# Kernel tuning notes

Measured on AMD Instinct MI355X. Metric: run time of the kernel, lower is better.

## Reference

```python
import jax, jax.numpy as jnp
import numpy as np

CDECAY = 0.5      # NEURON_CDECAY = 1/2
VDECAY = 0.75     # NEURON_VDECAY = 3/4
VTH_INIT = 0.5
T = 50            # batch_window
sg = jax.lax.stop_gradient


@jax.custom_vjp
def pseudo_spike(v, vth):
    return (v > vth).astype(v.dtype)

def _ps_fwd(v, vth):
    return pseudo_spike(v, vth), (v, vth)

def _ps_bwd(res, g):
    v, vth = res
    # PseudoSpikeRect: rectangular surrogate gradient, window 0.5; no grad to vth
    return (g * (jnp.abs(v - vth) < 0.5).astype(g.dtype), jnp.zeros_like(vth))

pseudo_spike.defvjp(_ps_fwd, _ps_bwd)


def lif_step(x_in, W, b, u, v_prev, s_prev, temporal):
    """One neuron_model_* call + the temporal-threshold update that follows it."""
    u = u * CDECAY + x_in @ W.T + b
    v = v_prev * VDECAY * (1.0 - s_prev) + u
    # energy threshold term uses detached volts in the original (numpy round-trip)
    energy = jnp.exp((sg(v_prev) - sg(v)) / 3.0) - 1.0
    vth = 0.5 * temporal + 0.5 * energy
    s = pseudo_spike(v, vth)
    vsg = sg(v)  # threshold chain never reaches the loss (custom fn has no vth grad)
    V_m = vsg.mean() - 0.2 * (vsg.max() - vsg.min())
    V_theta = vth.mean() - 0.2 * (vth.max() - vth.min())
    temporal_new = 0.01 * (vsg - V_m) + V_theta + jnp.log(1.0 + jnp.exp((vsg - V_m) / 4.0))
    return u, v, s, temporal_new


def _forward(x, fc1_u, fc1_v, fc1_s, fc2_u, fc2_v, fc2_s, fc3_u, fc3_v, fc3_s,
             fc4_u, fc4_v, fc4_s, W1, b1, W2, b2, W3, b3, W4, b4):
    B = x.shape[0]
    H = W1.shape[0]
    A = W4.shape[0]
    t1 = jnp.full((B, H), VTH_INIT, x.dtype)
    t2 = jnp.full((B, H), VTH_INIT, x.dtype)
    t3 = jnp.full((B, H), VTH_INIT, x.dtype)
    t4 = jnp.full((B, A), VTH_INIT, x.dtype)
    acc = jnp.zeros((B, A), x.dtype)
    xs = jnp.transpose(x, (2, 0, 1))  # [T, B, state_num]

    def step(carry, xt):
        (u1, v1, s1, tt1, u2, v2, s2, tt2, u3, v3, s3, tt3, u4, v4, s4, tt4, a) = carry
        u1, v1, s1, tt1 = lif_step(xt, W1, b1, u1, v1, s1, tt1)
        u2, v2, s2, tt2 = lif_step(s1, W2, b2, u2, v2, s2, tt2)
        u3, v3, s3, tt3 = lif_step(s2, W3, b3, u3, v3, s3, tt3)
        u4, v4, s4, tt4 = lif_step(s3, W4, b4, u4, v4, s4, tt4)
        a = a + s4
        return (u1, v1, s1, tt1, u2, v2, s2, tt2, u3, v3, s3, tt3, u4, v4, s4, tt4, a), None

    carry0 = (fc1_u, fc1_v, fc1_s, t1, fc2_u, fc2_v, fc2_s, t2,
              fc3_u, fc3_v, fc3_s, t3, fc4_u, fc4_v, fc4_s, t4, acc)
    carry, _ = jax.lax.scan(step, carry0, xs)
    return carry[-1] / T  # fc4_sumspike / batch_window


def setup_inputs() -> dict:
    key = jax.random.key(0)
    ks = jax.random.split(key, 10)
    B, S, H, A = 2048, 256, 256, 2
    inp = {"x": jax.random.normal(ks[0], (B, S, T), jnp.float32)}
    for name, shp in [("fc1_u", (B, H)), ("fc1_v", (B, H)), ("fc1_s", (B, H)),
                      ("fc2_u", (B, H)), ("fc2_v", (B, H)), ("fc2_s", (B, H)),
                      ("fc3_u", (B, H)), ("fc3_v", (B, H)), ("fc3_s", (B, H)),
                      ("fc4_u", (B, A)), ("fc4_v", (B, A)), ("fc4_s", (B, A))]:
        inp[name] = jnp.zeros(shp, jnp.float32)
    def lin(k, fan_out, fan_in):
        bound = 1.0 / np.sqrt(fan_in)
        kw, kb = jax.random.split(k)
        W = jax.random.uniform(kw, (fan_out, fan_in), jnp.float32, -bound, bound)
        b = jax.random.uniform(kb, (fan_out,), jnp.float32, -bound, bound)
        return W, b
    inp["W1"], inp["b1"] = lin(ks[1], H, S)
    inp["W2"], inp["b2"] = lin(ks[2], H, H)
    inp["W3"], inp["b3"] = lin(ks[3], H, H)
    inp["W4"], inp["b4"] = lin(ks[4], A, H)
    inp["batch_size"] = B
    return inp


def reference(x, fc1_u, fc1_v, fc1_s, fc2_u, fc2_v, fc2_s, fc3_u, fc3_v, fc3_s,
              fc4_u, fc4_v, fc4_s, W1, b1, W2, b2, W3, b3, W4, b4, batch_size):
    return _forward(x, fc1_u, fc1_v, fc1_s, fc2_u, fc2_v, fc2_s,
                    fc3_u, fc3_v, fc3_s, fc4_u, fc4_v, fc4_s,
                    W1, b1, W2, b2, W3, b3, W4, b4)
```

## Files before the change

kernel.cpp:

```cpp
#include <hip/hip_runtime.h>
#include <cstdint>
#include <cstddef>

#define BB 2048
#define SS 256
#define HH 256
#define AA 2
#define TT 50
#define ROWS  32
#define NTHR  512
#define NLG   64
#define NGRID 192
#define KSTR  272
#define WLAYER (256 * KSTR)
#define LSTR  36
#define S3P   260

struct Params {
  const float* x;
  const float* fu[3]; const float* fv[3]; const float* fs[3];
  const float* f4u; const float* f4v; const float* f4s;
  const float* W[3]; const float* bs[3];
  const float* W4; const float* b4;
  float* out;
  float* wt3;
  float* partials;
  unsigned* flags;
  float* sbuf;
  float* xT;
  int use_xt;
};

__device__ __forceinline__ void pstore(float* p, float v) {
  __hip_atomic_store(p, v, __ATOMIC_RELAXED, __HIP_MEMORY_SCOPE_AGENT);
}
__device__ __forceinline__ float pload(const float* p) {
  return __hip_atomic_load(p, __ATOMIC_RELAXED, __HIP_MEMORY_SCOPE_AGENT);
}
__device__ __forceinline__ unsigned uload_acq(const unsigned* p) {
  return __hip_atomic_load(p, __ATOMIC_ACQUIRE, __HIP_MEMORY_SCOPE_AGENT);
}
__device__ __forceinline__ void ustore_rel(unsigned* p, unsigned v) {
  __hip_atomic_store(p, v, __ATOMIC_RELEASE, __HIP_MEMORY_SCOPE_AGENT);
}
__device__ __forceinline__ void uadd(unsigned* p) {
  __hip_atomic_fetch_add(p, 1u, __ATOMIC_ACQ_REL, __HIP_MEMORY_SCOPE_AGENT);
}

#define OUTER(IV, WV)                                        \
  acc[0][0] = fmaf((IV).x, (WV).x, acc[0][0]);               \
  acc[0][1] = fmaf((IV).x, (WV).y, acc[0][1]);               \
  acc[0][2] = fmaf((IV).x, (WV).z, acc[0][2]);               \
  acc[0][3] = fmaf((IV).x, (WV).w, acc[0][3]);               \
  acc[1][0] = fmaf((IV).y, (WV).x, acc[1][0]);               \
  acc[1][1] = fmaf((IV).y, (WV).y, acc[1][1]);               \
  acc[1][2] = fmaf((IV).y, (WV).z, acc[1][2]);               \
  acc[1][3] = fmaf((IV).y, (WV).w, acc[1][3]);               \
  acc[2][0] = fmaf((IV).z, (WV).x, acc[2][0]);               \
  acc[2][1] = fmaf((IV).z, (WV).y, acc[2][1]);               \
  acc[2][2] = fmaf((IV).z, (WV).z, acc[2][2]);               \
  acc[2][3] = fmaf((IV).z, (WV).w, acc[2][3]);               \
  acc[3][0] = fmaf((IV).w, (WV).x, acc[3][0]);               \
  acc[3][1] = fmaf((IV).w, (WV).y, acc[3][1]);               \
  acc[3][2] = fmaf((IV).w, (WV).z, acc[3][2]);               \
  acc[3][3] = fmaf((IV).w, (WV).w, acc[3][3]);

__global__ __launch_bounds__(NTHR, 2)
void snn_pipe(Params p) {
#pragma clang fp contract(off)
  const int tid = threadIdx.x;
  const int blk = blockIdx.x;
  const int L   = blk >> 6;
  const int g   = blk & 63;
  const int B0  = g * ROWS;

  const int w    = tid >> 6;
  const int l    = tid & 63;
  const int hp   = w & 3;
  const int qp   = w >> 2;
  const int hsel = l & 15;
  const int jsel = l >> 4;
  const int hb   = hp * 64 + hsel * 4;
  const int jb   = qp * 16 + jsel * 4;

  const int sid = tid & 255;
  const int jq  = tid >> 8;

  __shared__ __align__(16) float in_lds[HH * LSTR];
  __shared__ __align__(16) float s3_lds[ROWS * S3P];
  __shared__ float wred[8][6];
  __shared__ float scal[2][2];
  __shared__ float l4u[64], l4v[64], l4s[64], l4t[64],
                   l4acc[64], l4vn[64], l4vth[64];

  {
    const int gtid = blk * NTHR + tid;
    if (gtid < 16384) {
      const int h = gtid & 255, kq = gtid >> 8;
      #pragma unroll
      for (int ll = 0; ll < 3; ++ll) {
        float4 wv = *reinterpret_cast<const float4*>(p.W[ll] + (size_t)h * 256 + kq * 4);
        float* dst = p.wt3 + (size_t)ll * WLAYER + (size_t)(kq * 4) * KSTR + h;
        dst[0 * KSTR] = wv.x; dst[1 * KSTR] = wv.y;
        dst[2 * KSTR] = wv.z; dst[3 * KSTR] = wv.w;
      }
    }
    if (p.use_xt) {
      for (int sid0 = gtid; sid0 < BB * SS; sid0 += NGRID * NTHR) {
        const float* src = p.x + (size_t)sid0 * TT;
        #pragma unroll 1
        for (int t = 0; t < TT; ++t)
          p.xT[(size_t)t * (BB * SS) + sid0] = src[t];
      }
    }
  }

  float u[4][4], v[4][4], tp[4][4];
  unsigned smask = 0;
  #pragma unroll
  for (int jj = 0; jj < 4; ++jj) {
    size_t idx = (size_t)(B0 + jb + jj) * HH + hb;
    float4 uu = *reinterpret_cast<const float4*>(p.fu[L] + idx);
    float4 vv = *reinterpret_cast<const float4*>(p.fv[L] + idx);
    float4 ss = *reinterpret_cast<const float4*>(p.fs[L] + idx);
    u[jj][0] = uu.x; u[jj][1] = uu.y; u[jj][2] = uu.z; u[jj][3] = uu.w;
    v[jj][0] = vv.x; v[jj][1] = vv.y; v[jj][2] = vv.z; v[jj][3] = vv.w;
    if (ss.x != 0.0f) smask |= 1u << (jj * 4 + 0);
    if (ss.y != 0.0f) smask |= 1u << (jj * 4 + 1);
    if (ss.z != 0.0f) smask |= 1u << (jj * 4 + 2);
    if (ss.w != 0.0f) smask |= 1u << (jj * 4 + 3);
    #pragma unroll
    for (int i = 0; i < 4; ++i) tp[jj][i] = 0.5f;
  }
  const float4 bb4 = *reinterpret_cast<const float4*>(p.bs[L] + hb);
  const float bL[4] = { bb4.x, bb4.y, bb4.z, bb4.w };
  if (L == 2 && tid < 64) {
    size_t idx = (size_t)(B0 + (tid >> 1)) * AA + (tid & 1);
    l4u[tid] = p.f4u[idx]; l4v[tid] = p.f4v[idx]; l4s[tid] = p.f4s[idx];
    l4t[tid] = 0.5f; l4acc[tid] = 0.0f;
  }
  __syncthreads();

  if (tid == 0) {
    uadd(&p.flags[260]);
    while (uload_acq(&p.flags[260]) < (unsigned)NGRID) __builtin_amdgcn_s_sleep(2);
  }
  __syncthreads();

  const float* wbase = p.wt3 + (size_t)L * WLAYER + hb;
  float* sb_in  = (L > 0) ? p.sbuf + (size_t)(L - 1) * 2 * BB * HH : nullptr;
  float* sb_out = (L < 2) ? p.sbuf + (size_t)L * 2 * BB * HH : nullptr;

  #pragma unroll 1
  for (int t = 0; t < TT; ++t) {
    if (L == 0) {
      if (p.use_xt) {
        const float* base = p.xT + (size_t)t * (BB * SS) + (size_t)B0 * SS;
        #pragma unroll
        for (int iq = 0; iq < 4; ++iq) {
          const int j = jq * 16 + iq * 4;
          float4 vv = make_float4(base[(size_t)(j + 0) * SS + sid],
                                  base[(size_t)(j + 1) * SS + sid],
                                  base[(size_t)(j + 2) * SS + sid],
                                  base[(size_t)(j + 3) * SS + sid]);
          *reinterpret_cast<float4*>(&in_lds[sid * LSTR + j]) = vv;
        }
      } else {
        #pragma unroll
        for (int iq = 0; iq < 4; ++iq) {
          const int j = jq * 16 + iq * 4;
          float4 vv = make_float4(
              p.x[((size_t)(B0 + j + 0) * SS + sid) * TT + t],
              p.x[((size_t)(B0 + j + 1) * SS + sid) * TT + t],
              p.x[((size_t)(B0 + j + 2) * SS + sid) * TT + t],
              p.x[((size_t)(B0 + j + 3) * SS + sid) * TT + t]);
          *reinterpret_cast<float4*>(&in_lds[sid * LSTR + j]) = vv;
        }
      }
    } else {
      const int hop = L - 1;
      if (tid == 0) {
        while (uload_acq(&p.flags[hop * 64 + g]) < (unsigned)(t + 1))
          __builtin_amdgcn_s_sleep(2);
      }
      __syncthreads();
      const float* src = sb_in + (size_t)(t & 1) * BB * HH;
      #pragma unroll
      for (int iq = 0; iq < 4; ++iq) {
        const int j = jq * 16 + iq * 4;
        float4 vv = make_float4(pload(src + (size_t)(B0 + j + 0) * HH + sid),
                                pload(src + (size_t)(B0 + j + 1) * HH + sid),
                                pload(src + (size_t)(B0 + j + 2) * HH + sid),
                                pload(src + (size_t)(B0 + j + 3) * HH + sid));
        *reinterpret_cast<float4*>(&in_lds[sid * LSTR + j]) = vv;
      }
      __syncthreads();
      if (tid == 0) ustore_rel(&p.flags[128 + hop * 64 + g], (unsigned)(t + 1));
    }
    __syncthreads();

    float acc[4][4];
    #pragma unroll
    for (int jj = 0; jj < 4; ++jj)
      #pragma unroll
      for (int i = 0; i < 4; ++i) acc[jj][i] = 0.0f;
    #pragma unroll 2
    for (int k4 = 0; k4 < 64; ++k4) {
      const float* wk = wbase + (size_t)(k4 * 4) * KSTR;
      float4 w0 = *reinterpret_cast<const float4*>(wk);
      float4 w1 = *reinterpret_cast<const float4*>(wk + KSTR);
      float4 w2 = *reinterpret_cast<const float4*>(wk + 2 * KSTR);
      float4 w3 = *reinterpret_cast<const float4*>(wk + 3 * KSTR);
      const float* ib = &in_lds[(k4 * 4) * LSTR + jb];
      float4 i0 = *reinterpret_cast<const float4*>(ib);
      float4 i1 = *reinterpret_cast<const float4*>(ib + LSTR);
      float4 i2 = *reinterpret_cast<const float4*>(ib + 2 * LSTR);
      float4 i3 = *reinterpret_cast<const float4*>(ib + 3 * LSTR);
      OUTER(i0, w0);
      OUTER(i1, w1);
      OUTER(i2, w2);
      OUTER(i3, w3);
    }

    if (t > 0) {
      if (tid == 0) {
        while (uload_acq(&p.flags[256 + L]) < (unsigned)(NLG * t))
          __builtin_amdgcn_s_sleep(2);
      }
      __syncthreads();
      {
        const int wv = tid >> 6, ln = tid & 63;
        if (wv == 0 || (wv == 1 && L == 2)) {
          const int ch = (wv == 0) ? L : 3;
          const float* pb = p.partials + (size_t)(ch * 2 + ((t - 1) & 1)) * 6 * 64;
          float r[6];
          #pragma unroll
          for (int st = 0; st < 6; ++st) {
            float rr = pload(pb + st * 64 + ln);
            if (st == 0 || st == 3) {
              #pragma unroll
              for (int m = 1; m < 64; m <<= 1) rr += __shfl_xor(rr, m);
            } else if (st == 1 || st == 4) {
              #pragma unroll
              for (int m = 1; m < 64; m <<= 1) rr = fmaxf(rr, __shfl_xor(rr, m));
            } else {
              #pragma unroll
              for (int m = 1; m < 64; m <<= 1) rr = fminf(rr, __shfl_xor(rr, m));
            }
            r[st] = rr;
          }
          if (ln == 0) {
            const float invN = (ch == 3) ? (1.0f / 4096.0f) : (1.0f / 524288.0f);
            scal[wv][0] = (r[0] * invN) - 0.2f * (r[1] - r[2]);
            scal[wv][1] = (r[3] * invN) - 0.2f * (r[4] - r[5]);
          }
        }
      }
      __syncthreads();
      {
        const float Vm = scal[0][0], Vt = scal[0][1];
        #pragma unroll
        for (int jj = 0; jj < 4; ++jj)
          #pragma unroll
          for (int i = 0; i < 4; ++i) {
            float d = v[jj][i] - Vm;
            float sp = logf(1.0f + expf(d * 0.25f));
            tp[jj][i] = (0.01f * d + Vt) + sp;
          }
      }
      if (L == 2 && tid < 64) {
        const float Vm = scal[1][0], Vt = scal[1][1];
        float d = l4v[tid] - Vm;
        float sp = logf(1.0f + expf(d * 0.25f));
        l4t[tid] = (0.01f * d + Vt) + sp;
      }
      __syncthreads();
    }

    float sv = 0.f, svt = 0.f;
    float mxv = -3.402823466e38f, mnv = 3.402823466e38f;
    float mxvt = -3.402823466e38f, mnvt = 3.402823466e38f;
    unsigned nsmask = 0;
    #pragma unroll
    for (int jj = 0; jj < 4; ++jj) {
      #pragma unroll
      for (int i = 0; i < 4; ++i) {
        float un = fmaf(u[jj][i], 0.5f, acc[jj][i]) + bL[i];
        float vp = v[jj][i];
        float vd = ((smask >> (jj * 4 + i)) & 1u) ? 0.0f : vp * 0.75f;
        float vn = vd + un;
        float en = expf((vp - vn) / 3.0f) - 1.0f;
        float vt = 0.5f * tp[jj][i] + 0.5f * en;
        const bool sx = vn > vt;
        u[jj][i] = un; v[jj][i] = vn;
        if (sx) nsmask |= 1u << (jj * 4 + i);
        sv += vn; svt += vt;
        mxv = fmaxf(mxv, vn); mnv = fminf(mnv, vn);
        mxvt = fmaxf(mxvt, vt); mnvt = fminf(mnvt, vt);
      }
    }
    smask = nsmask;
    #pragma unroll
    for (int m = 1; m < 64; m <<= 1) {
      sv += __shfl_xor(sv, m);   svt += __shfl_xor(svt, m);
      mxv = fmaxf(mxv, __shfl_xor(mxv, m));  mnv = fminf(mnv, __shfl_xor(mnv, m));
      mxvt = fmaxf(mxvt, __shfl_xor(mxvt, m)); mnvt = fminf(mnvt, __shfl_xor(mnvt, m));
    }
    if ((tid & 63) == 0) {
      int wv = tid >> 6;
      wred[wv][0] = sv;  wred[wv][1] = mxv;  wred[wv][2] = mnv;
      wred[wv][3] = svt; wred[wv][4] = mxvt; wred[wv][5] = mnvt;
    }
    #pragma unroll
    for (int jj = 0; jj < 4; ++jj) {
      *reinterpret_cast<float4*>(&s3_lds[(jb + jj) * S3P + hb]) = make_float4(
          ((nsmask >> (jj * 4 + 0)) & 1u) ? 1.0f : 0.0f,
          ((nsmask >> (jj * 4 + 1)) & 1u) ? 1.0f : 0.0f,
          ((nsmask >> (jj * 4 + 2)) & 1u) ? 1.0f : 0.0f,
          ((nsmask >> (jj * 4 + 3)) & 1u) ? 1.0f : 0.0f);
    }
    __syncthreads();

    if (L < 2) {
      if (tid < 6) {
        const int st = tid;
        float r = wred[0][st];
        if (st == 0 || st == 3) {
          #pragma unroll
          for (int wv = 1; wv < 8; ++wv) r = r + wred[wv][st];
        } else if (st == 1 || st == 4) {
          #pragma unroll
          for (int wv = 1; wv < 8; ++wv) r = fmaxf(r, wred[wv][st]);
        } else {
          #pragma unroll
          for (int wv = 1; wv < 8; ++wv) r = fminf(r, wred[wv][st]);
        }
        pstore(p.partials + (size_t)(L * 2 + (t & 1)) * 6 * 64 + st * 64 + g, r);
      }
      if (t >= 2 && tid == 1) {
        while (uload_acq(&p.flags[128 + L * 64 + g]) < (unsigned)(t - 1))
          __builtin_amdgcn_s_sleep(2);
      }
      __syncthreads();
      if (tid == 0) uadd(&p.flags[256 + L]);
      float* dst = sb_out + (size_t)(t & 1) * BB * HH;
      #pragma unroll
      for (int jr = 0; jr < 16; ++jr) {
        const int j = jq * 16 + jr;
        pstore(dst + (size_t)(B0 + j) * HH + sid, s3_lds[j * S3P + sid]);
      }
      __syncthreads();
      if (tid == 0) ustore_rel(&p.flags[L * 64 + g], (unsigned)(t + 1));
    } else {
      if (tid < 6) {
        const int st = tid;
        float r = wred[0][st];
        if (st == 0 || st == 3) {
          #pragma unroll
          for (int wv = 1; wv < 8; ++wv) r = r + wred[wv][st];
        } else if (st == 1 || st == 4) {
          #pragma unroll
          for (int wv = 1; wv < 8; ++wv) r = fmaxf(r, wred[wv][st]);
        } else {
          #pragma unroll
          for (int wv = 1; wv < 8; ++wv) r = fminf(r, wred[wv][st]);
        }
        pstore(p.partials + (size_t)(2 * 2 + (t & 1)) * 6 * 64 + st * 64 + g, r);
      }
      __syncthreads();

      {
        const int d = tid >> 3, c = tid & 7;
        if (d < 64) {
          const int j4 = d >> 1, a4 = d & 1;
          float part = 0.0f;
          #pragma unroll
          for (int i = 0; i < 32; ++i) {
            int k = c + 8 * i;
            part = fmaf(s3_lds[j4 * S3P + k], p.W4[a4 * HH + k], part);
          }
          #pragma unroll
          for (int m = 1; m < 8; m <<= 1) part += __shfl_xor(part, m);
          if (c == 0) {
            float un = fmaf(l4u[d], 0.5f, part) + p.b4[a4];
            float vp = l4v[d];
            float vd = (vp * 0.75f) * (1.0f - l4s[d]);
            float vn = vd + un;
            float en = expf((vp - vn) / 3.0f) - 1.0f;
            float vt = 0.5f * l4t[d] + 0.5f * en;
            float sx = (vn > vt) ? 1.0f : 0.0f;
            l4u[d] = un; l4v[d] = vn; l4s[d] = sx;
            l4acc[d] += sx; l4vn[d] = vn; l4vth[d] = vt;
          }
        }
      }
      __syncthreads();

      if (tid < 64) {
        float a = l4vn[tid], b = l4vth[tid];
        float s4 = a, mx4 = a, mn4 = a;
        float st4 = b, mxt4 = b, mnt4 = b;
        #pragma unroll
        for (int m = 1; m < 64; m <<= 1) {
          s4  += __shfl_xor(s4, m);   st4 += __shfl_xor(st4, m);
          mx4  = fmaxf(mx4,  __shfl_xor(mx4, m));  mn4  = fminf(mn4,  __shfl_xor(mn4, m));
          mxt4 = fmaxf(mxt4, __shfl_xor(mxt4, m)); mnt4 = fminf(mnt4, __shfl_xor(mnt4, m));
        }
        if (tid == 0) {
          float* pp = p.partials + (size_t)(3 * 2 + (t & 1)) * 6 * 64 + g;
          pstore(pp + 0 * 64, s4);   pstore(pp + 1 * 64, mx4);  pstore(pp + 2 * 64, mn4);
          pstore(pp + 3 * 64, st4);  pstore(pp + 4 * 64, mxt4); pstore(pp + 5 * 64, mnt4);
        }
      }
      __syncthreads();
      if (tid == 0) uadd(&p.flags[256 + L]);
    }
  }

  if (L == 2 && tid < 64)
    p.out[(size_t)(B0 + (tid >> 1)) * AA + (tid & 1)] = l4acc[tid] / 50.0f;
}

extern "C" void kernel_launch(void* const* d_in, const int* in_sizes, int n_in,
                              void* d_out, int out_size, void* d_ws, size_t ws_size,
                              hipStream_t stream) {
  Params p;
  p.x     = (const float*)d_in[0];
  p.fu[0] = (const float*)d_in[1];  p.fv[0] = (const float*)d_in[2];  p.fs[0] = (const float*)d_in[3];
  p.fu[1] = (const float*)d_in[4];  p.fv[1] = (const float*)d_in[5];  p.fs[1] = (const float*)d_in[6];
  p.fu[2] = (const float*)d_in[7];  p.fv[2] = (const float*)d_in[8];  p.fs[2] = (const float*)d_in[9];
  p.f4u   = (const float*)d_in[10]; p.f4v   = (const float*)d_in[11]; p.f4s   = (const float*)d_in[12];
  p.W[0]  = (const float*)d_in[13]; p.bs[0] = (const float*)d_in[14];
  p.W[1]  = (const float*)d_in[15]; p.bs[1] = (const float*)d_in[16];
  p.W[2]  = (const float*)d_in[17]; p.bs[2] = (const float*)d_in[18];
  p.W4    = (const float*)d_in[19]; p.b4    = (const float*)d_in[20];
  p.out   = (float*)d_out;

  float* ws   = (float*)d_ws;
  p.wt3       = ws;
  p.partials  = ws + 208896;
  p.flags     = (unsigned*)(ws + 211968);
  p.sbuf      = ws + 212992;
  p.xT        = ws + 2310144;
  size_t need = ((size_t)2310144 + (size_t)TT * BB * SS) * sizeof(float);
  p.use_xt    = (ws_size >= need) ? 1 : 0;

  hipMemsetAsync((void*)p.flags, 0, 4096, stream);
  snn_pipe<<<dim3(NGRID), dim3(NTHR), 0, stream>>>(p);
}
```

Baseline: 1.890 ms.

## Halve rows per block and double grid to 384 persistent blocks

Each block now processes 16 batch rows instead of 32, so the grid grows to 128 blocks per layer (384 in total) and launch bounds request 4 blocks per CU. The per-thread register tile shrinks from 4x4 to 2x4, and flags, partials and the cross-block reductions are resized and re-indexed for 128 groups. The aim is to spread the per-timestep GEMM and pipeline work across more CUs and cut serial work per block. In exchange the weights are re-read from global memory by twice as many blocks, there are more flag and atomic synchronisations per step, and all 384 persistent blocks must be co-resident for the spin barriers to avoid deadlock.

```diff
diff --git a/kernel.cpp b/kernel.cpp
--- a/kernel.cpp
+++ b/kernel.cpp
@@ -7,13 +7,13 @@
 #define HH 256
 #define AA 2
 #define TT 50
-#define ROWS  32
+#define ROWS  16
 #define NTHR  512
-#define NLG   64
-#define NGRID 192
+#define NLG   128
+#define NGRID 384
 #define KSTR  272
 #define WLAYER (256 * KSTR)
-#define LSTR  36
+#define LSTR  20
 #define S3P   260
 
 struct Params {
@@ -47,7 +47,7 @@
   __hip_atomic_fetch_add(p, 1u, __ATOMIC_ACQ_REL, __HIP_MEMORY_SCOPE_AGENT);
 }
 
-#define OUTER(IV, WV)                                        \
+#define OUTER2(IV, WV)                                       \
   acc[0][0] = fmaf((IV).x, (WV).x, acc[0][0]);               \
   acc[0][1] = fmaf((IV).x, (WV).y, acc[0][1]);               \
   acc[0][2] = fmaf((IV).x, (WV).z, acc[0][2]);               \
@@ -55,23 +55,15 @@
   acc[1][0] = fmaf((IV).y, (WV).x, acc[1][0]);               \
   acc[1][1] = fmaf((IV).y, (WV).y, acc[1][1]);               \
   acc[1][2] = fmaf((IV).y, (WV).z, acc[1][2]);               \
-  acc[1][3] = fmaf((IV).y, (WV).w, acc[1][3]);               \
-  acc[2][0] = fmaf((IV).z, (WV).x, acc[2][0]);               \
-  acc[2][1] = fmaf((IV).z, (WV).y, acc[2][1]);               \
-  acc[2][2] = fmaf((IV).z, (WV).z, acc[2][2]);               \
-  acc[2][3] = fmaf((IV).z, (WV).w, acc[2][3]);               \
-  acc[3][0] = fmaf((IV).w, (WV).x, acc[3][0]);               \
-  acc[3][1] = fmaf((IV).w, (WV).y, acc[3][1]);               \
-  acc[3][2] = fmaf((IV).w, (WV).z, acc[3][2]);               \
-  acc[3][3] = fmaf((IV).w, (WV).w, acc[3][3]);
-
-__global__ __launch_bounds__(NTHR, 2)
+  acc[1][3] = fmaf((IV).y, (WV).w, acc[1][3]);
+
+__global__ __launch_bounds__(NTHR, 4)
 void snn_pipe(Params p) {
 #pragma clang fp contract(off)
   const int tid = threadIdx.x;
   const int blk = blockIdx.x;
-  const int L   = blk >> 6;
-  const int g   = blk & 63;
+  const int L   = blk >> 7;
+  const int g   = blk & 127;
   const int B0  = g * ROWS;
 
   const int w    = tid >> 6;
@@ -81,7 +73,7 @@
   const int hsel = l & 15;
   const int jsel = l >> 4;
   const int hb   = hp * 64 + hsel * 4;
-  const int jb   = qp * 16 + jsel * 4;
+  const int jb   = qp * 8 + jsel * 2;
 
   const int sid = tid & 255;
   const int jq  = tid >> 8;
@@ -90,8 +82,8 @@
   __shared__ __align__(16) float s3_lds[ROWS * S3P];
   __shared__ float wred[8][6];
   __shared__ float scal[2][2];
-  __shared__ float l4u[64], l4v[64], l4s[64], l4t[64],
-                   l4acc[64], l4vn[64], l4vth[64];
+  __shared__ float l4u[32], l4v[32], l4s[32], l4t[32],
+                   l4acc[32], l4vn[32], l4vth[32];
 
   {
     const int gtid = blk * NTHR + tid;
@@ -115,10 +107,10 @@
     }
   }
 
-  float u[4][4], v[4][4], tp[4][4];
+  float u[2][4], v[2][4], tp[2][4];
   unsigned smask = 0;
   #pragma unroll
-  for (int jj = 0; jj < 4; ++jj) {
+  for (int jj = 0; jj < 2; ++jj) {
     size_t idx = (size_t)(B0 + jb + jj) * HH + hb;
     float4 uu = *reinterpret_cast<const float4*>(p.fu[L] + idx);
     float4 vv = *reinterpret_cast<const float4*>(p.fv[L] + idx);
@@ -134,7 +126,7 @@
   }
   const float4 bb4 = *reinterpret_cast<const float4*>(p.bs[L] + hb);
   const float bL[4] = { bb4.x, bb4.y, bb4.z, bb4.w };
-  if (L == 2 && tid < 64) {
+  if (L == 2 && tid < 32) {
     size_t idx = (size_t)(B0 + (tid >> 1)) * AA + (tid & 1);
     l4u[tid] = p.f4u[idx]; l4v[tid] = p.f4v[idx]; l4s[tid] = p.f4s[idx];
     l4t[tid] = 0.5f; l4acc[tid] = 0.0f;
@@ -142,8 +134,8 @@
   __syncthreads();
 
   if (tid == 0) {
-    uadd(&p.flags[260]);
-    while (uload_acq(&p.flags[260]) < (unsigned)NGRID) __builtin_amdgcn_s_sleep(2);
+    uadd(&p.flags[516]);
+    while (uload_acq(&p.flags[516]) < (unsigned)NGRID) __builtin_amdgcn_s_sleep(2);
   }
   __syncthreads();
 
@@ -157,8 +149,8 @@
       if (p.use_xt) {
         const float* base = p.xT + (size_t)t * (BB * SS) + (size_t)B0 * SS;
         #pragma unroll
-        for (int iq = 0; iq < 4; ++iq) {
-          const int j = jq * 16 + iq * 4;
+        for (int iq = 0; iq < 2; ++iq) {
+          const int j = jq * 8 + iq * 4;
           float4 vv = make_float4(base[(size_t)(j + 0) * SS + sid],
                                   base[(size_t)(j + 1) * SS + sid],
                                   base[(size_t)(j + 2) * SS + sid],
@@ -167,8 +159,8 @@
         }
       } else {
         #pragma unroll
-        for (int iq = 0; iq < 4; ++iq) {
-          const int j = jq * 16 + iq * 4;
+        for (int iq = 0; iq < 2; ++iq) {
+          const int j = jq * 8 + iq * 4;
           float4 vv = make_float4(
               p.x[((size_t)(B0 + j + 0) * SS + sid) * TT + t],
               p.x[((size_t)(B0 + j + 1) * SS + sid) * TT + t],
@@ -180,14 +172,14 @@
     } else {
       const int hop = L - 1;
       if (tid == 0) {
-        while (uload_acq(&p.flags[hop * 64 + g]) < (unsigned)(t + 1))
+        while (uload_acq(&p.flags[hop * 128 + g]) < (unsigned)(t + 1))
           __builtin_amdgcn_s_sleep(2);
       }
       __syncthreads();
       const float* src = sb_in + (size_t)(t & 1) * BB * HH;
       #pragma unroll
-      for (int iq = 0; iq < 4; ++iq) {
-        const int j = jq * 16 + iq * 4;
+      for (int iq = 0; iq < 2; ++iq) {
+        const int j = jq * 8 + iq * 4;
         float4 vv = make_float4(pload(src + (size_t)(B0 + j + 0) * HH + sid),
                                 pload(src + (size_t)(B0 + j + 1) * HH + sid),
                                 pload(src + (size_t)(B0 + j + 2) * HH + sid),
@@ -195,13 +187,13 @@
         *reinterpret_cast<float4*>(&in_lds[sid * LSTR + j]) = vv;
       }
       __syncthreads();
-      if (tid == 0) ustore_rel(&p.flags[128 + hop * 64 + g], (unsigned)(t + 1));
+      if (tid == 0) ustore_rel(&p.flags[256 + hop * 128 + g], (unsigned)(t + 1));
     }
     __syncthreads();
 
-    float acc[4][4];
+    float acc[2][4];
     #pragma unroll
-    for (int jj = 0; jj < 4; ++jj)
+    for (int jj = 0; jj < 2; ++jj)
       #pragma unroll
       for (int i = 0; i < 4; ++i) acc[jj][i] = 0.0f;
     #pragma unroll 2
@@ -212,19 +204,19 @@
       float4 w2 = *reinterpret_cast<const float4*>(wk + 2 * KSTR);
       float4 w3 = *reinterpret_cast<const float4*>(wk + 3 * KSTR);
       const float* ib = &in_lds[(k4 * 4) * LSTR + jb];
-      float4 i0 = *reinterpret_cast<const float4*>(ib);
-      float4 i1 = *reinterpret_cast<const float4*>(ib + LSTR);
-      float4 i2 = *reinterpret_cast<const float4*>(ib + 2 * LSTR);
-      float4 i3 = *reinterpret_cast<const float4*>(ib + 3 * LSTR);
-      OUTER(i0, w0);
-      OUTER(i1, w1);
-      OUTER(i2, w2);
-      OUTER(i3, w3);
+      float2 i0 = *reinterpret_cast<const float2*>(ib);
+      float2 i1 = *reinterpret_cast<const float2*>(ib + LSTR);
+      float2 i2 = *reinterpret_cast<const float2*>(ib + 2 * LSTR);
+      float2 i3 = *reinterpret_cast<const float2*>(ib + 3 * LSTR);
+      OUTER2(i0, w0);
+      OUTER2(i1, w1);
+      OUTER2(i2, w2);
+      OUTER2(i3, w3);
     }
 
     if (t > 0) {
       if (tid == 0) {
-        while (uload_acq(&p.flags[256 + L]) < (unsigned)(NLG * t))
+        while (uload_acq(&p.flags[512 + L]) < (unsigned)(NLG * t))
           __builtin_amdgcn_s_sleep(2);
       }
       __syncthreads();
@@ -232,18 +224,23 @@
         const int wv = tid >> 6, ln = tid & 63;
         if (wv == 0 || (wv == 1 && L == 2)) {
           const int ch = (wv == 0) ? L : 3;
-          const float* pb = p.partials + (size_t)(ch * 2 + ((t - 1) & 1)) * 6 * 64;
+          const float* pb = p.partials + (size_t)(ch * 2 + ((t - 1) & 1)) * 6 * NLG;
           float r[6];
           #pragma unroll
           for (int st = 0; st < 6; ++st) {
-            float rr = pload(pb + st * 64 + ln);
+            const float* q = pb + st * NLG;
+            float a0 = pload(q + ln), a1 = pload(q + ln + 64);
+            float rr;
             if (st == 0 || st == 3) {
+              rr = a0 + a1;
               #pragma unroll
               for (int m = 1; m < 64; m <<= 1) rr += __shfl_xor(rr, m);
             } else if (st == 1 || st == 4) {
+              rr = fmaxf(a0, a1);
               #pragma unroll
               for (int m = 1; m < 64; m <<= 1) rr = fmaxf(rr, __shfl_xor(rr, m));
             } else {
+              rr = fminf(a0, a1);
               #pragma unroll
               for (int m = 1; m < 64; m <<= 1) rr = fminf(rr, __shfl_xor(rr, m));
             }
@@ -260,7 +257,7 @@
       {
         const float Vm = scal[0][0], Vt = scal[0][1];
         #pragma unroll
-        for (int jj = 0; jj < 4; ++jj)
+        for (int jj = 0; jj < 2; ++jj)
           #pragma unroll
           for (int i = 0; i < 4; ++i) {
             float d = v[jj][i] - Vm;
@@ -268,7 +265,7 @@
             tp[jj][i] = (0.01f * d + Vt) + sp;
           }
       }
-      if (L == 2 && tid < 64) {
+      if (L == 2 && tid < 32) {
         const float Vm = scal[1][0], Vt = scal[1][1];
         float d = l4v[tid] - Vm;
         float sp = logf(1.0f + expf(d * 0.25f));
@@ -282,7 +279,7 @@
     float mxvt = -3.402823466e38f, mnvt = 3.402823466e38f;
     unsigned nsmask = 0;
     #pragma unroll
-    for (int jj = 0; jj < 4; ++jj) {
+    for (int jj = 0; jj < 2; ++jj) {
       #pragma unroll
       for (int i = 0; i < 4; ++i) {
         float un = fmaf(u[jj][i], 0.5f, acc[jj][i]) + bL[i];
@@ -312,7 +309,7 @@
       wred[wv][3] = svt; wred[wv][4] = mxvt; wred[wv][5] = mnvt;
     }
     #pragma unroll
-    for (int jj = 0; jj < 4; ++jj) {
+    for (int jj = 0; jj < 2; ++jj) {
       *reinterpret_cast<float4*>(&s3_lds[(jb + jj) * S3P + hb]) = make_float4(
           ((nsmask >> (jj * 4 + 0)) & 1u) ? 1.0f : 0.0f,
           ((nsmask >> (jj * 4 + 1)) & 1u) ? 1.0f : 0.0f,
@@ -335,22 +332,22 @@
           #pragma unroll
           for (int wv = 1; wv < 8; ++wv) r = fminf(r, wred[wv][st]);
         }
-        pstore(p.partials + (size_t)(L * 2 + (t & 1)) * 6 * 64 + st * 64 + g, r);
+        pstore(p.partials + (size_t)(L * 2 + (t & 1)) * 6 * NLG + st * NLG + g, r);
       }
       if (t >= 2 && tid == 1) {
-        while (uload_acq(&p.flags[128 + L * 64 + g]) < (unsigned)(t - 1))
+        while (uload_acq(&p.flags[256 + L * 128 + g]) < (unsigned)(t - 1))
           __builtin_amdgcn_s_sleep(2);
       }
       __syncthreads();
-      if (tid == 0) uadd(&p.flags[256 + L]);
+      if (tid == 0) uadd(&p.flags[512 + L]);
       float* dst = sb_out + (size_t)(t & 1) * BB * HH;
       #pragma unroll
-      for (int jr = 0; jr < 16; ++jr) {
-        const int j = jq * 16 + jr;
+      for (int jr = 0; jr < 8; ++jr) {
+        const int j = jq * 8 + jr;
         pstore(dst + (size_t)(B0 + j) * HH + sid, s3_lds[j * S3P + sid]);
       }
       __syncthreads();
-      if (tid == 0) ustore_rel(&p.flags[L * 64 + g], (unsigned)(t + 1));
+      if (tid == 0) ustore_rel(&p.flags[L * 128 + g], (unsigned)(t + 1));
     } else {
       if (tid < 6) {
         const int st = tid;
@@ -365,22 +362,22 @@
           #pragma unroll
           for (int wv = 1; wv < 8; ++wv) r = fminf(r, wred[wv][st]);
         }
-        pstore(p.partials + (size_t)(2 * 2 + (t & 1)) * 6 * 64 + st * 64 + g, r);
+        pstore(p.partials + (size_t)(2 * 2 + (t & 1)) * 6 * NLG + st * NLG + g, r);
       }
       __syncthreads();
 
       {
-        const int d = tid >> 3, c = tid & 7;
-        if (d < 64) {
+        const int d = tid >> 4, c = tid & 15;
+        if (d < 32) {
           const int j4 = d >> 1, a4 = d & 1;
           float part = 0.0f;
           #pragma unroll
-          for (int i = 0; i < 32; ++i) {
-            int k = c + 8 * i;
+          for (int i = 0; i < 16; ++i) {
+            int k = c + 16 * i;
             part = fmaf(s3_lds[j4 * S3P + k], p.W4[a4 * HH + k], part);
           }
           #pragma unroll
-          for (int m = 1; m < 8; m <<= 1) part += __shfl_xor(part, m);
+          for (int m = 1; m < 16; m <<= 1) part += __shfl_xor(part, m);
           if (c == 0) {
             float un = fmaf(l4u[d], 0.5f, part) + p.b4[a4];
             float vp = l4v[d];
@@ -396,28 +393,28 @@
       }
       __syncthreads();
 
-      if (tid < 64) {
+      if (tid < 32) {
         float a = l4vn[tid], b = l4vth[tid];
         float s4 = a, mx4 = a, mn4 = a;
         float st4 = b, mxt4 = b, mnt4 = b;
         #pragma unroll
-        for (int m = 1; m < 64; m <<= 1) {
+        for (int m = 1; m < 32; m <<= 1) {
           s4  += __shfl_xor(s4, m);   st4 += __shfl_xor(st4, m);
           mx4  = fmaxf(mx4,  __shfl_xor(mx4, m));  mn4  = fminf(mn4,  __shfl_xor(mn4, m));
           mxt4 = fmaxf(mxt4, __shfl_xor(mxt4, m)); mnt4 = fminf(mnt4, __shfl_xor(mnt4, m));
         }
         if (tid == 0) {
-          float* pp = p.partials + (size_t)(3 * 2 + (t & 1)) * 6 * 64 + g;
-          pstore(pp + 0 * 64, s4);   pstore(pp + 1 * 64, mx4);  pstore(pp + 2 * 64, mn4);
-          pstore(pp + 3 * 64, st4);  pstore(pp + 4 * 64, mxt4); pstore(pp + 5 * 64, mnt4);
-        }
-      }
-      __syncthreads();
-      if (tid == 0) uadd(&p.flags[256 + L]);
+          float* pp = p.partials + (size_t)(3 * 2 + (t & 1)) * 6 * NLG + g;
+          pstore(pp + 0 * NLG, s4);   pstore(pp + 1 * NLG, mx4);  pstore(pp + 2 * NLG, mn4);
+          pstore(pp + 3 * NLG, st4);  pstore(pp + 4 * NLG, mxt4); pstore(pp + 5 * NLG, mnt4);
+        }
+      }
+      __syncthreads();
+      if (tid == 0) uadd(&p.flags[512 + L]);
     }
   }
 
-  if (L == 2 && tid < 64)
+  if (L == 2 && tid < 32)
     p.out[(size_t)(B0 + (tid >> 1)) * AA + (tid & 1)] = l4acc[tid] / 50.0f;
 }
 
@@ -439,10 +436,10 @@
   float* ws   = (float*)d_ws;
   p.wt3       = ws;
   p.partials  = ws + 208896;
-  p.flags     = (unsigned*)(ws + 211968);
-  p.sbuf      = ws + 212992;
-  p.xT        = ws + 2310144;
-  size_t need = ((size_t)2310144 + (size_t)TT * BB * SS) * sizeof(float);
+  p.flags     = (unsigned*)(ws + 215040);
+  p.sbuf      = ws + 216064;
+  p.xT        = ws + 2313216;
+  size_t need = ((size_t)2313216 + (size_t)TT * BB * SS) * sizeof(float);
   p.use_xt    = (ws_size >= need) ? 1 : 0;
 
   hipMemsetAsync((void*)p.flags, 0, 4096, stream);
```

After: 4.347 ms. 130% more time.

## Use last-arriver reduction, byte spike buffers, and 4-deep inter-layer ring

Applied to the files above, without the earlier changes.

The last block to increment the per-layer counter now finishes the global mean/max/min reduction and publishes two scalars plus a flag. Other blocks wait on that flag and read the two scalars instead of each re-reducing all 64 partials. Inter-layer spike buffers become uint8 instead of float, cutting the traffic between layers by four. The ring buffer also deepens from 2 to 4 slots, which loosens producer back-pressure. The cost is more atomic-ordering complexity and a serial tail in the last-arriving block.

```diff
diff --git a/kernel.cpp b/kernel.cpp
--- a/kernel.cpp
+++ b/kernel.cpp
@@ -25,8 +25,9 @@
   float* out;
   float* wt3;
   float* partials;
+  float* scal_g;
   unsigned* flags;
-  float* sbuf;
+  uint8_t* sbuf;
   float* xT;
   int use_xt;
 };
@@ -37,14 +38,20 @@
 __device__ __forceinline__ float pload(const float* p) {
   return __hip_atomic_load(p, __ATOMIC_RELAXED, __HIP_MEMORY_SCOPE_AGENT);
 }
+__device__ __forceinline__ void bstore(uint8_t* p, uint8_t v) {
+  __hip_atomic_store(p, v, __ATOMIC_RELAXED, __HIP_MEMORY_SCOPE_AGENT);
+}
+__device__ __forceinline__ uint8_t bload(const uint8_t* p) {
+  return __hip_atomic_load(p, __ATOMIC_RELAXED, __HIP_MEMORY_SCOPE_AGENT);
+}
 __device__ __forceinline__ unsigned uload_acq(const unsigned* p) {
   return __hip_atomic_load(p, __ATOMIC_ACQUIRE, __HIP_MEMORY_SCOPE_AGENT);
 }
 __device__ __forceinline__ void ustore_rel(unsigned* p, unsigned v) {
   __hip_atomic_store(p, v, __ATOMIC_RELEASE, __HIP_MEMORY_SCOPE_AGENT);
 }
-__device__ __forceinline__ void uadd(unsigned* p) {
-  __hip_atomic_fetch_add(p, 1u, __ATOMIC_ACQ_REL, __HIP_MEMORY_SCOPE_AGENT);
+__device__ __forceinline__ unsigned uadd_ret(unsigned* p) {
+  return __hip_atomic_fetch_add(p, 1u, __ATOMIC_ACQ_REL, __HIP_MEMORY_SCOPE_AGENT);
 }
 
 #define OUTER(IV, WV)                                        \
@@ -142,17 +149,18 @@
   __syncthreads();
 
   if (tid == 0) {
-    uadd(&p.flags[260]);
+    uadd_ret(&p.flags[260]);
     while (uload_acq(&p.flags[260]) < (unsigned)NGRID) __builtin_amdgcn_s_sleep(2);
   }
   __syncthreads();
 
   const float* wbase = p.wt3 + (size_t)L * WLAYER + hb;
-  float* sb_in  = (L > 0) ? p.sbuf + (size_t)(L - 1) * 2 * BB * HH : nullptr;
-  float* sb_out = (L < 2) ? p.sbuf + (size_t)L * 2 * BB * HH : nullptr;
+  uint8_t* sb_in  = (L > 0) ? p.sbuf + (size_t)(L - 1) * 4 * BB * HH : nullptr;
+  uint8_t* sb_out = (L < 2) ? p.sbuf + (size_t)L * 4 * BB * HH : nullptr;
 
   #pragma unroll 1
   for (int t = 0; t < TT; ++t) {
+    const int par = t & 1;
     if (L == 0) {
       if (p.use_xt) {
         const float* base = p.xT + (size_t)t * (BB * SS) + (size_t)B0 * SS;
@@ -184,14 +192,15 @@
           __builtin_amdgcn_s_sleep(2);
       }
       __syncthreads();
-      const float* src = sb_in + (size_t)(t & 1) * BB * HH;
+      const uint8_t* src = sb_in + (size_t)(t & 3) * BB * HH;
       #pragma unroll
       for (int iq = 0; iq < 4; ++iq) {
         const int j = jq * 16 + iq * 4;
-        float4 vv = make_float4(pload(src + (size_t)(B0 + j + 0) * HH + sid),
-                                pload(src + (size_t)(B0 + j + 1) * HH + sid),
-                                pload(src + (size_t)(B0 + j + 2) * HH + sid),
-                                pload(src + (size_t)(B0 + j + 3) * HH + sid));
+        float4 vv = make_float4(
+            (float)bload(src + (size_t)(B0 + j + 0) * HH + sid),
+            (float)bload(src + (size_t)(B0 + j + 1) * HH + sid),
+            (float)bload(src + (size_t)(B0 + j + 2) * HH + sid),
+            (float)bload(src + (size_t)(B0 + j + 3) * HH + sid));
         *reinterpret_cast<float4*>(&in_lds[sid * LSTR + j]) = vv;
       }
       __syncthreads();
@@ -224,36 +233,14 @@
 
     if (t > 0) {
       if (tid == 0) {
-        while (uload_acq(&p.flags[256 + L]) < (unsigned)(NLG * t))
+        while (uload_acq(&p.flags[264 + L]) < (unsigned)t)
           __builtin_amdgcn_s_sleep(2);
-      }
-      __syncthreads();
-      {
-        const int wv = tid >> 6, ln = tid & 63;
-        if (wv == 0 || (wv == 1 && L == 2)) {
-          const int ch = (wv == 0) ? L : 3;
-          const float* pb = p.partials + (size_t)(ch * 2 + ((t - 1) & 1)) * 6 * 64;
-          float r[6];
-          #pragma unroll
-          for (int st = 0; st < 6; ++st) {
-            float rr = pload(pb + st * 64 + ln);
-            if (st == 0 || st == 3) {
-              #pragma unroll
-              for (int m = 1; m < 64; m <<= 1) rr += __shfl_xor(rr, m);
-            } else if (st == 1 || st == 4) {
-              #pragma unroll
-              for (int m = 1; m < 64; m <<= 1) rr = fmaxf(rr, __shfl_xor(rr, m));
-            } else {
-              #pragma unroll
-              for (int m = 1; m < 64; m <<= 1) rr = fminf(rr, __shfl_xor(rr, m));
-            }
-            r[st] = rr;
-          }
-          if (ln == 0) {
-            const float invN = (ch == 3) ? (1.0f / 4096.0f) : (1.0f / 524288.0f);
-            scal[wv][0] = (r[0] * invN) - 0.2f * (r[1] - r[2]);
-            scal[wv][1] = (r[3] * invN) - 0.2f * (r[4] - r[5]);
-          }
+        const int pp = (t - 1) & 1;
+        scal[0][0] = pload(p.scal_g + (size_t)(L * 2 + pp) * 2 + 0);
+        scal[0][1] = pload(p.scal_g + (size_t)(L * 2 + pp) * 2 + 1);
+        if (L == 2) {
+          scal[1][0] = pload(p.scal_g + (size_t)(3 * 2 + pp) * 2 + 0);
+          scal[1][1] = pload(p.scal_g + (size_t)(3 * 2 + pp) * 2 + 1);
         }
       }
       __syncthreads();
@@ -322,98 +309,166 @@
     __syncthreads();
 
     if (L < 2) {
-      if (tid < 6) {
-        const int st = tid;
-        float r = wred[0][st];
-        if (st == 0 || st == 3) {
+      if (w == 0) {
+        if (l < 6) {
+          const int st = l;
+          float r = wred[0][st];
+          if (st == 0 || st == 3) {
+            #pragma unroll
+            for (int wv = 1; wv < 8; ++wv) r = r + wred[wv][st];
+          } else if (st == 1 || st == 4) {
+            #pragma unroll
+            for (int wv = 1; wv < 8; ++wv) r = fmaxf(r, wred[wv][st]);
+          } else {
+            #pragma unroll
+            for (int wv = 1; wv < 8; ++wv) r = fminf(r, wred[wv][st]);
+          }
+          pstore(p.partials + (size_t)(L * 2 + par) * 6 * 64 + st * 64 + g, r);
+        }
+        int islast = 0;
+        if (l == 0) {
+          unsigned old = uadd_ret(&p.flags[256 + L]);
+          islast = (old == (unsigned)(NLG * (t + 1) - 1));
+        }
+        islast = __shfl(islast, 0);
+        if (islast) {
+          const float* pb = p.partials + (size_t)(L * 2 + par) * 6 * 64;
+          float r[6];
           #pragma unroll
-          for (int wv = 1; wv < 8; ++wv) r = r + wred[wv][st];
-        } else if (st == 1 || st == 4) {
-          #pragma unroll
-          for (int wv = 1; wv < 8; ++wv) r = fmaxf(r, wred[wv][st]);
-        } else {
-          #pragma unroll
-          for (int wv = 1; wv < 8; ++wv) r = fminf(r, wred[wv][st]);
-        }
-        pstore(p.partials + (size_t)(L * 2 + (t & 1)) * 6 * 64 + st * 64 + g, r);
-      }
-      if (t >= 2 && tid == 1) {
-        while (uload_acq(&p.flags[128 + L * 64 + g]) < (unsigned)(t - 1))
+          for (int st = 0; st < 6; ++st) {
+            float rr = pload(pb + st * 64 + l);
+            if (st == 0 || st == 3) {
+              #pragma unroll
+              for (int m = 1; m < 64; m <<= 1) rr += __shfl_xor(rr, m);
+            } else if (st == 1 || st == 4) {
+              #pragma unroll
+              for (int m = 1; m < 64; m <<= 1) rr = fmaxf(rr, __shfl_xor(rr, m));
+            } else {
+              #pragma unroll
+              for (int m = 1; m < 64; m <<= 1) rr = fminf(rr, __shfl_xor(rr, m));
+            }
+            r[st] = rr;
+          }
+          if (l == 0) {
+            const float invN = 1.0f / 524288.0f;
+            pstore(p.scal_g + (size_t)(L * 2 + par) * 2 + 0,
+                   (r[0] * invN) - 0.2f * (r[1] - r[2]));
+            pstore(p.scal_g + (size_t)(L * 2 + par) * 2 + 1,
+                   (r[3] * invN) - 0.2f * (r[4] - r[5]));
+            ustore_rel(&p.flags[264 + L], (unsigned)(t + 1));
+          }
+        }
+      }
+      if (t >= 4 && tid == 64) {
+        while (uload_acq(&p.flags[128 + L * 64 + g]) < (unsigned)(t - 2))
           __builtin_amdgcn_s_sleep(2);
       }
       __syncthreads();
-      if (tid == 0) uadd(&p.flags[256 + L]);
-      float* dst = sb_out + (size_t)(t & 1) * BB * HH;
+      uint8_t* dst = sb_out + (size_t)(t & 3) * BB * HH;
       #pragma unroll
       for (int jr = 0; jr < 16; ++jr) {
         const int j = jq * 16 + jr;
-        pstore(dst + (size_t)(B0 + j) * HH + sid, s3_lds[j * S3P + sid]);
+        bstore(dst + (size_t)(B0 + j) * HH + sid,
+               (uint8_t)(s3_lds[j * S3P + sid] != 0.0f ? 1 : 0));
       }
       __syncthreads();
       if (tid == 0) ustore_rel(&p.flags[L * 64 + g], (unsigned)(t + 1));
     } else {
-      if (tid < 6) {
-        const int st = tid;
-        float r = wred[0][st];
-        if (st == 0 || st == 3) {
-          #pragma unroll
-          for (int wv = 1; wv < 8; ++wv) r = r + wred[wv][st];
-        } else if (st == 1 || st == 4) {
-          #pragma unroll
-          for (int wv = 1; wv < 8; ++wv) r = fmaxf(r, wred[wv][st]);
-        } else {
-          #pragma unroll
-          for (int wv = 1; wv < 8; ++wv) r = fminf(r, wred[wv][st]);
-        }
-        pstore(p.partials + (size_t)(2 * 2 + (t & 1)) * 6 * 64 + st * 64 + g, r);
-      }
-      __syncthreads();
-
       {
         const int d = tid >> 3, c = tid & 7;
-        if (d < 64) {
-          const int j4 = d >> 1, a4 = d & 1;
-          float part = 0.0f;
+        const int j4 = d >> 1, a4 = d & 1;
+        float part = 0.0f;
+        #pragma unroll
+        for (int i = 0; i < 32; ++i) {
+          int k = c + 8 * i;
+          part = fmaf(s3_lds[j4 * S3P + k], p.W4[a4 * HH + k], part);
+        }
+        #pragma unroll
+        for (int m = 1; m < 8; m <<= 1) part += __shfl_xor(part, m);
+        if (c == 0) {
+          float un = fmaf(l4u[d], 0.5f, part) + p.b4[a4];
+          float vp = l4v[d];
+          float vd = (vp * 0.75f) * (1.0f - l4s[d]);
+          float vn = vd + un;
+          float en = expf((vp - vn) / 3.0f) - 1.0f;
+          float vt = 0.5f * l4t[d] + 0.5f * en;
+          float sx = (vn > vt) ? 1.0f : 0.0f;
+          l4u[d] = un; l4v[d] = vn; l4s[d] = sx;
+          l4acc[d] += sx; l4vn[d] = vn; l4vth[d] = vt;
+        }
+      }
+      __syncthreads();
+
+      if (w == 0) {
+        if (l < 6) {
+          const int st = l;
+          float r = wred[0][st];
+          if (st == 0 || st == 3) {
+            #pragma unroll
+            for (int wv = 1; wv < 8; ++wv) r = r + wred[wv][st];
+          } else if (st == 1 || st == 4) {
+            #pragma unroll
+            for (int wv = 1; wv < 8; ++wv) r = fmaxf(r, wred[wv][st]);
+          } else {
+            #pragma unroll
+            for (int wv = 1; wv < 8; ++wv) r = fminf(r, wred[wv][st]);
+          }
+          pstore(p.partials + (size_t)(2 * 2 + par) * 6 * 64 + st * 64 + g, r);
+        }
+        {
+          float a = l4vn[l], b = l4vth[l];
+          float s4 = a, mx4 = a, mn4 = a;
+          float st4 = b, mxt4 = b, mnt4 = b;
           #pragma unroll
-          for (int i = 0; i < 32; ++i) {
-            int k = c + 8 * i;
-            part = fmaf(s3_lds[j4 * S3P + k], p.W4[a4 * HH + k], part);
-          }
+          for (int m = 1; m < 64; m <<= 1) {
+            s4  += __shfl_xor(s4, m);   st4 += __shfl_xor(st4, m);
+            mx4  = fmaxf(mx4,  __shfl_xor(mx4, m));  mn4  = fminf(mn4,  __shfl_xor(mn4, m));
+            mxt4 = fmaxf(mxt4, __shfl_xor(mxt4, m)); mnt4 = fminf(mnt4, __shfl_xor(mnt4, m));
+          }
+          if (l == 0) {
+            float* pp = p.partials + (size_t)(3 * 2 + par) * 6 * 64 + g;
+            pstore(pp + 0 * 64, s4);   pstore(pp + 1 * 64, mx4);  pstore(pp + 2 * 64, mn4);
+            pstore(pp + 3 * 64, st4);  pstore(pp + 4 * 64, mxt4); pstore(pp + 5 * 64, mnt4);
+          }
+        }
+        int islast = 0;
+        if (l == 0) {
+          unsigned old = uadd_ret(&p.flags[256 + 2]);
+          islast = (old == (unsigned)(NLG * (t + 1) - 1));
+        }
+        islast = __shfl(islast, 0);
+        if (islast) {
           #pragma unroll
-          for (int m = 1; m < 8; m <<= 1) part += __shfl_xor(part, m);
-          if (c == 0) {
-            float un = fmaf(l4u[d], 0.5f, part) + p.b4[a4];
-            float vp = l4v[d];
-            float vd = (vp * 0.75f) * (1.0f - l4s[d]);
-            float vn = vd + un;
-            float en = expf((vp - vn) / 3.0f) - 1.0f;
-            float vt = 0.5f * l4t[d] + 0.5f * en;
-            float sx = (vn > vt) ? 1.0f : 0.0f;
-            l4u[d] = un; l4v[d] = vn; l4s[d] = sx;
-            l4acc[d] += sx; l4vn[d] = vn; l4vth[d] = vt;
-          }
-        }
-      }
-      __syncthreads();
-
-      if (tid < 64) {
-        float a = l4vn[tid], b = l4vth[tid];
-        float s4 = a, mx4 = a, mn4 = a;
-        float st4 = b, mxt4 = b, mnt4 = b;
-        #pragma unroll
-        for (int m = 1; m < 64; m <<= 1) {
-          s4  += __shfl_xor(s4, m);   st4 += __shfl_xor(st4, m);
-          mx4  = fmaxf(mx4,  __shfl_xor(mx4, m));  mn4  = fminf(mn4,  __shfl_xor(mn4, m));
-          mxt4 = fmaxf(mxt4, __shfl_xor(mxt4, m)); mnt4 = fminf(mnt4, __shfl_xor(mnt4, m));
-        }
-        if (tid == 0) {
-          float* pp = p.partials + (size_t)(3 * 2 + (t & 1)) * 6 * 64 + g;
-          pstore(pp + 0 * 64, s4);   pstore(pp + 1 * 64, mx4);  pstore(pp + 2 * 64, mn4);
-          pstore(pp + 3 * 64, st4);  pstore(pp + 4 * 64, mxt4); pstore(pp + 5 * 64, mnt4);
-        }
-      }
-      __syncthreads();
-      if (tid == 0) uadd(&p.flags[256 + L]);
+          for (int ch = 2; ch <= 3; ++ch) {
+            const float* pb = p.partials + (size_t)(ch * 2 + par) * 6 * 64;
+            float r[6];
+            #pragma unroll
+            for (int st = 0; st < 6; ++st) {
+              float rr = pload(pb + st * 64 + l);
+              if (st == 0 || st == 3) {
+                #pragma unroll
+                for (int m = 1; m < 64; m <<= 1) rr += __shfl_xor(rr, m);
+              } else if (st == 1 || st == 4) {
+                #pragma unroll
+                for (int m = 1; m < 64; m <<= 1) rr = fmaxf(rr, __shfl_xor(rr, m));
+              } else {
+                #pragma unroll
+                for (int m = 1; m < 64; m <<= 1) rr = fminf(rr, __shfl_xor(rr, m));
+              }
+              r[st] = rr;
+            }
+            if (l == 0) {
+              const float invN = (ch == 3) ? (1.0f / 4096.0f) : (1.0f / 524288.0f);
+              pstore(p.scal_g + (size_t)(ch * 2 + par) * 2 + 0,
+                     (r[0] * invN) - 0.2f * (r[1] - r[2]));
+              pstore(p.scal_g + (size_t)(ch * 2 + par) * 2 + 1,
+                     (r[3] * invN) - 0.2f * (r[4] - r[5]));
+            }
+          }
+          if (l == 0) ustore_rel(&p.flags[264 + 2], (unsigned)(t + 1));
+        }
+      }
+      __syncthreads();
     }
   }
 
@@ -439,10 +494,11 @@
   float* ws   = (float*)d_ws;
   p.wt3       = ws;
   p.partials  = ws + 208896;
-  p.flags     = (unsigned*)(ws + 211968);
-  p.sbuf      = ws + 212992;
-  p.xT        = ws + 2310144;
-  size_t need = ((size_t)2310144 + (size_t)TT * BB * SS) * sizeof(float);
+  p.scal_g    = ws + 211968;
+  p.flags     = (unsigned*)(ws + 212032);
+  p.sbuf      = (uint8_t*)(ws + 213056);
+  p.xT        = ws + 1261632;
+  size_t need = ((size_t)1261632 + (size_t)TT * BB * SS) * sizeof(float);
   p.use_xt    = (ws_size >= need) ? 1 : 0;
 
   hipMemsetAsync((void*)p.flags, 0, 4096, stream);
```

Measured after the change: 2.018 ms. +6.8%, slower.
